# Optimization experiments

Measured on AMD Instinct MI355X. Metric: run time of the kernel, lower is better.

The kernel has to match this reference:

```python
import jax, jax.numpy as jnp
import numpy as np

BATCH = 262144
NUM_CLASSES = 1000
K = 0.5
T = 3.0
ALPHA = 1.0
GAMMA = 2.0
# error_weights dict: {(i, (i+1) % NUM_CLASSES): 2.0 for i in range(100)}
ERROR_WEIGHTS = {(i, (i + 1) % NUM_CLASSES): 2.0 for i in range(100)}


def setup_inputs() -> dict:
    key = jax.random.key(0)
    k1, k2 = jax.random.split(key)
    output = jax.random.normal(k1, (BATCH, NUM_CLASSES), dtype=jnp.float32)
    target = jax.random.randint(k2, (BATCH,), 0, NUM_CLASSES)
    wt = np.zeros((NUM_CLASSES, NUM_CLASSES), dtype=np.float32)
    mk = np.zeros((NUM_CLASSES, NUM_CLASSES), dtype=bool)
    for (t_, p_), w in ERROR_WEIGHTS.items():
        wt[t_, p_] = w
        mk[t_, p_] = True
    return {
        "output": output,
        "target": target,
        "weight_table": jnp.asarray(wt),
        "in_dict": jnp.asarray(mk),
    }


def reference(output, target, weight_table, in_dict):
    b = output.shape[0]
    # per-sample cross entropy (stable log-softmax)
    logp = jax.nn.log_softmax(output, axis=-1)                     # [B, C]
    ce = -jnp.take_along_axis(logp, target[:, None], axis=1)[:, 0]  # [B]
    pt = jnp.exp(-ce)
    f_loss = ALPHA * (1.0 - pt) ** GAMMA * ce                      # [B]
    pred = jnp.argmax(output, axis=-1)                             # [B]
    # dense-table lookup replacing the per-sample Python dict loop
    w = weight_table[target, pred]                                 # [B]
    m = in_dict[target, pred]                                      # [B] bool
    loss1 = jnp.sum(jnp.where(m, f_loss * w, 0.0))
    loss2 = jnp.sum(jnp.where(m, 0.0, f_loss))
    l1 = loss1 / b
    l2 = loss2 / b
    w2 = jax.nn.sigmoid(K * (jax.lax.stop_gradient(l1) - T))
    total = jnp.where(loss1 > 0, l1 + w2 * l2, loss2 / b)
    return total
```

## Files before the change

### kernel.cpp

```cpp
#include <hip/hip_runtime.h>
#include <math.h>

#define BATCH 262144
#define NUM_CLASSES 1000

__global__ __launch_bounds__(256) void dbfl_main(
    const float* __restrict__ output,
    const int* __restrict__ target,
    const float* __restrict__ wt,
    double* __restrict__ acc)
{
    const int lane = threadIdx.x & 63;
    const int wib  = threadIdx.x >> 6;
    const int wpb  = blockDim.x >> 6;
    const long long gwave  = (long long)blockIdx.x * wpb + wib;
    const long long nwaves = (long long)gridDim.x * wpb;

    float acc1 = 0.f, acc2 = 0.f;

    for (long long row = gwave; row < BATCH; row += nwaves) {
        const float* rp = output + row * (long long)NUM_CLASSES;
        const float4* rp4 = (const float4*)rp;

        float4 v[4];
#pragma unroll
        for (int c = 0; c < 4; ++c) {
            int f = lane + 64 * c;
            if (f < NUM_CLASSES / 4) {
                v[c] = rp4[f];
            } else {
                v[c] = make_float4(-INFINITY, -INFINITY, -INFINITY, -INFINITY);
            }
        }

        float bm = -INFINITY; int bi = NUM_CLASSES;
#pragma unroll
        for (int c = 0; c < 4; ++c) {
            const int base = (lane + 64 * c) * 4;
            const float vv[4] = {v[c].x, v[c].y, v[c].z, v[c].w};
#pragma unroll
            for (int j = 0; j < 4; ++j) {
                const float x = vv[j]; const int col = base + j;
                if (x > bm || (x == bm && col < bi)) { bm = x; bi = col; }
            }
        }

        float wm = bm; int wi = bi;
#pragma unroll
        for (int off = 32; off > 0; off >>= 1) {
            float om = __shfl_xor(wm, off, 64);
            int   oi = __shfl_xor(wi, off, 64);
            if (om > wm || (om == wm && oi < wi)) { wm = om; wi = oi; }
        }

        float s = 0.f;
#pragma unroll
        for (int c = 0; c < 4; ++c) {
            s += __expf(v[c].x - wm);
            s += __expf(v[c].y - wm);
            s += __expf(v[c].z - wm);
            s += __expf(v[c].w - wm);
        }
#pragma unroll
        for (int off = 32; off > 0; off >>= 1)
            s += __shfl_xor(s, off, 64);

        if (lane == 0) {
            const int t  = target[row];
            const float xt = rp[t];
            const float ce = wm + __logf(s) - xt;
            const float pt = __expf(-ce);
            const float om_pt = 1.f - pt;
            const float fl = om_pt * om_pt * ce;
            const float w  = wt[t * NUM_CLASSES + wi];
            if (w != 0.f) acc1 += fl * w;
            else          acc2 += fl;
        }
    }

    __shared__ float sh1[8], sh2[8];
    if (lane == 0) { sh1[wib] = acc1; sh2[wib] = acc2; }
    __syncthreads();
    if (threadIdx.x == 0) {
        float a = 0.f, b = 0.f;
        for (int i = 0; i < wpb; ++i) { a += sh1[i]; b += sh2[i]; }
        unsafeAtomicAdd(&acc[0], (double)a);
        unsafeAtomicAdd(&acc[1], (double)b);
    }
}

__global__ void dbfl_final(const double* __restrict__ acc, float* __restrict__ out)
{
    const double loss1 = acc[0];
    const double loss2 = acc[1];
    const double b  = (double)BATCH;
    const double l1 = loss1 / b;
    const double l2 = loss2 / b;
    const double w2 = 1.0 / (1.0 + exp(-0.5 * (l1 - 3.0)));
    const double total = (loss1 > 0.0) ? (l1 + w2 * l2) : l2;
    out[0] = (float)total;
}

extern "C" void kernel_launch(void* const* d_in, const int* in_sizes, int n_in,
                              void* d_out, int out_size, void* d_ws, size_t ws_size,
                              hipStream_t stream)
{
    const float* output = (const float*)d_in[0];
    const int*   target = (const int*)d_in[1];
    const float* wt     = (const float*)d_in[2];

    double* acc = (double*)d_ws;
    hipMemsetAsync(d_ws, 0, 2 * sizeof(double), stream);

    const int block = 256;
    const int grid  = 2048;
    dbfl_main<<<grid, block, 0, stream>>>(output, target, wt, acc);
    dbfl_final<<<1, 1, 0, stream>>>(acc, (float*)d_out);
}
```

Baseline: 1.313 ms.

## Software-pipeline row loads and simplify argmax/target-logit extraction with shuffles

Restructures the per-wave row loop to prefetch the next row's logits and target into registers while the current row is reduced, overlapping global-memory latency with compute. It also splits argmax into a max reduction followed by a min-index reduction, reads the target logit from registers via a wave shuffle instead of a dependent global load, and issues the weight-table lookup with wave-uniform indices. Launch bounds gain a minimum-blocks hint. Double-buffering raises register pressure, which could reduce occupancy.

```diff
diff --git a/kernel.cpp b/kernel.cpp
--- a/kernel.cpp
+++ b/kernel.cpp
@@ -3,8 +3,9 @@
 
 #define BATCH 262144
 #define NUM_CLASSES 1000
+#define NF4 250
 
-__global__ __launch_bounds__(256) void dbfl_main(
+__global__ __launch_bounds__(256, 4) void dbfl_main(
     const float* __restrict__ output,
     const int* __restrict__ target,
     const float* __restrict__ wt,
@@ -18,63 +19,101 @@
 
     float acc1 = 0.f, acc2 = 0.f;
 
-    for (long long row = gwave; row < BATCH; row += nwaves) {
-        const float* rp = output + row * (long long)NUM_CLASSES;
-        const float4* rp4 = (const float4*)rp;
-
-        float4 v[4];
+    long long row = gwave;
+    if (row < BATCH) {
+        const float4* rp4 = (const float4*)(output + row * (long long)NUM_CLASSES);
+        float4 vc[4];
 #pragma unroll
         for (int c = 0; c < 4; ++c) {
-            int f = lane + 64 * c;
-            if (f < NUM_CLASSES / 4) {
-                v[c] = rp4[f];
-            } else {
-                v[c] = make_float4(-INFINITY, -INFINITY, -INFINITY, -INFINITY);
+            const int f = lane + 64 * c;
+            vc[c] = (f < NF4) ? rp4[f]
+                              : make_float4(-INFINITY, -INFINITY, -INFINITY, -INFINITY);
+        }
+        int tcur = target[row];
+
+        for (;;) {
+            const long long nrow = row + nwaves;
+            const bool have_next = (nrow < BATCH);
+            float4 vn[4];
+            int tnext = 0;
+            if (have_next) {
+                const float4* np4 = (const float4*)(output + nrow * (long long)NUM_CLASSES);
+#pragma unroll
+                for (int c = 0; c < 4; ++c) {
+                    const int f = lane + 64 * c;
+                    vn[c] = (f < NF4) ? np4[f]
+                                      : make_float4(-INFINITY, -INFINITY, -INFINITY, -INFINITY);
+                }
+                tnext = target[nrow];
             }
-        }
 
-        float bm = -INFINITY; int bi = NUM_CLASSES;
+            float bm = -INFINITY;
 #pragma unroll
-        for (int c = 0; c < 4; ++c) {
-            const int base = (lane + 64 * c) * 4;
-            const float vv[4] = {v[c].x, v[c].y, v[c].z, v[c].w};
+            for (int c = 0; c < 4; ++c)
+                bm = fmaxf(bm, fmaxf(fmaxf(vc[c].x, vc[c].y), fmaxf(vc[c].z, vc[c].w)));
+            float wm = bm;
 #pragma unroll
-            for (int j = 0; j < 4; ++j) {
-                const float x = vv[j]; const int col = base + j;
-                if (x > bm || (x == bm && col < bi)) { bm = x; bi = col; }
+            for (int off = 32; off > 0; off >>= 1)
+                wm = fmaxf(wm, __shfl_xor(wm, off, 64));
+
+            int bi = 0x7fffffff;
+#pragma unroll
+            for (int c = 3; c >= 0; --c) {
+                const int base = (lane + 64 * c) * 4;
+                if (vc[c].w == wm) bi = base + 3;
+                if (vc[c].z == wm) bi = base + 2;
+                if (vc[c].y == wm) bi = base + 1;
+                if (vc[c].x == wm) bi = base + 0;
             }
-        }
+            int wi = bi;
+#pragma unroll
+            for (int off = 32; off > 0; off >>= 1)
+                wi = min(wi, __shfl_xor(wi, off, 64));
 
-        float wm = bm; int wi = bi;
+            const int t_s  = __builtin_amdgcn_readfirstlane(tcur);
+            const int wi_s = __builtin_amdgcn_readfirstlane(wi);
+            const float w = wt[(long long)t_s * NUM_CLASSES + wi_s];
+
+            float s = 0.f;
 #pragma unroll
-        for (int off = 32; off > 0; off >>= 1) {
-            float om = __shfl_xor(wm, off, 64);
-            int   oi = __shfl_xor(wi, off, 64);
-            if (om > wm || (om == wm && oi < wi)) { wm = om; wi = oi; }
-        }
+            for (int c = 0; c < 4; ++c) {
+                s += __expf(vc[c].x - wm);
+                s += __expf(vc[c].y - wm);
+                s += __expf(vc[c].z - wm);
+                s += __expf(vc[c].w - wm);
+            }
+#pragma unroll
+            for (int off = 32; off > 0; off >>= 1)
+                s += __shfl_xor(s, off, 64);
 
-        float s = 0.f;
-#pragma unroll
-        for (int c = 0; c < 4; ++c) {
-            s += __expf(v[c].x - wm);
-            s += __expf(v[c].y - wm);
-            s += __expf(v[c].z - wm);
-            s += __expf(v[c].w - wm);
-        }
-#pragma unroll
-        for (int off = 32; off > 0; off >>= 1)
-            s += __shfl_xor(s, off, 64);
+            const int f4  = t_s >> 2;
+            const int src = f4 & 63;
+            const int ch  = f4 >> 6;
+            const int cm  = t_s & 3;
+            float4 vsel = vc[0];
+            if (ch == 1) vsel = vc[1];
+            else if (ch == 2) vsel = vc[2];
+            else if (ch == 3) vsel = vc[3];
+            float cand = vsel.x;
+            if (cm == 1) cand = vsel.y;
+            else if (cm == 2) cand = vsel.z;
+            else if (cm == 3) cand = vsel.w;
+            const float xt = __shfl(cand, src, 64);
 
-        if (lane == 0) {
-            const int t  = target[row];
-            const float xt = rp[t];
             const float ce = wm + __logf(s) - xt;
             const float pt = __expf(-ce);
             const float om_pt = 1.f - pt;
             const float fl = om_pt * om_pt * ce;
-            const float w  = wt[t * NUM_CLASSES + wi];
-            if (w != 0.f) acc1 += fl * w;
-            else          acc2 += fl;
+            if (lane == 0) {
+                if (w != 0.f) acc1 += fl * w;
+                else          acc2 += fl;
+            }
+
+            if (!have_next) break;
+#pragma unroll
+            for (int c = 0; c < 4; ++c) vc[c] = vn[c];
+            tcur = tnext;
+            row  = nrow;
         }
     }
 
```

Result: no change. 1.314 ms (+0.0%).
